# Performance work log

Measured on AMD Instinct MI355X. Metric: run time of the kernel, lower is better.

Reference implementation:

```python
import jax, jax.numpy as jnp
import numpy as np

D_MODEL = 64
HIDDEN = 64
N_HEADS = 4
HEAD_DIM = HIDDEN // N_HEADS  # 16
MAX_LEN = 128
LN_EPS = 1e-5


def setup_inputs() -> dict:
    key = jax.random.key(0)
    ks = jax.random.split(key, 16)
    B, Lh, Lp = 4096, 128, 32
    s = 0.02
    return {
        "hla_out": jax.random.normal(ks[0], (B, Lh, D_MODEL), jnp.float32),
        "pep_out": jax.random.normal(ks[1], (B, Lp, D_MODEL), jnp.float32),
        "W_hla": jax.random.normal(ks[2], (D_MODEL, HIDDEN), jnp.float32) * s,
        "b_hla": jnp.zeros((HIDDEN,), jnp.float32),
        "W_pep": jax.random.normal(ks[3], (D_MODEL, HIDDEN), jnp.float32) * s,
        "b_pep": jnp.zeros((HIDDEN,), jnp.float32),
        "rel_bias": jax.random.normal(ks[4], (N_HEADS, MAX_LEN, MAX_LEN), jnp.float32) * s,
        "ln_g": jnp.ones((HIDDEN,), jnp.float32),
        "ln_b": jnp.zeros((HIDDEN,), jnp.float32),
        "W1": jax.random.normal(ks[5], (HIDDEN, 2 * HIDDEN), jnp.float32) * s,
        "b1": jnp.zeros((2 * HIDDEN,), jnp.float32),
        "W2": jax.random.normal(ks[6], (2 * HIDDEN, HIDDEN), jnp.float32) * s,
        "b2": jnp.zeros((HIDDEN,), jnp.float32),
        "W_out": jax.random.normal(ks[7], (HIDDEN, D_MODEL), jnp.float32) * s,
        "b_out": jnp.zeros((D_MODEL,), jnp.float32),
    }


def _layernorm(x, g, b):
    mu = jnp.mean(x, axis=-1, keepdims=True)
    var = jnp.mean(jnp.square(x - mu), axis=-1, keepdims=True)
    return (x - mu) * jax.lax.rsqrt(var + LN_EPS) * g + b


def reference(hla_out, pep_out, W_hla, b_hla, W_pep, b_pep, rel_bias,
              ln_g, ln_b, W1, b1, W2, b2, W_out, b_out):
    B, Lh, _ = hla_out.shape
    Lp = pep_out.shape[1]
    hla = hla_out @ W_hla + b_hla              # [B, Lh, HIDDEN]
    pep = pep_out @ W_pep + b_pep              # [B, Lp, HIDDEN]
    q = hla.reshape(B, Lh, N_HEADS, HEAD_DIM)
    kv = pep.reshape(B, Lp, N_HEADS, HEAD_DIM)  # k and v share projection
    scale = 1.0 / np.sqrt(HEAD_DIM).astype(np.float32)
    # [B, H, Lh, Lp]
    scores = jnp.einsum('bqhd,bkhd->bhqk', q, kv) * scale
    scores = scores + rel_bias[:, :Lh, :Lp]
    attn = jax.nn.softmax(scores, axis=-1)
    ctx = jnp.einsum('bhqk,bkhd->bqhd', attn, kv).reshape(B, Lh, HIDDEN)
    h = _layernorm(ctx, ln_g, ln_b)
    h = jax.nn.gelu(h @ W1 + b1, approximate=False) @ W2 + b2
    hla2pep = hla + h                          # residual onto projected hla
    return hla2pep @ W_out + b_out             # [B, Lh, D_MODEL]
```

## Files before the change

kernel.cpp:

```cpp
#include <hip/hip_runtime.h>

#define DEV static __device__ __forceinline__

using bf16x8 = __attribute__((ext_vector_type(8))) short;
using f32x4  = __attribute__((ext_vector_type(4))) float;
using f32x16 = __attribute__((ext_vector_type(16))) float;
using bfp2   = __attribute__((ext_vector_type(2))) __bf16;
using u32x2  = __attribute__((ext_vector_type(2))) unsigned;

DEV unsigned short f2bf(float f){
  return __builtin_bit_cast(unsigned short, (__bf16)f);
}
DEV unsigned pk2(float a, float b){
  bfp2 v = {(__bf16)a, (__bf16)b};
  return __builtin_bit_cast(unsigned, v);
}
DEV void wr64(void* p, float a, float b, float c, float d){
  u32x2 v = {pk2(a, b), pk2(c, d)};
  *(u32x2*)p = v;
}

DEV float gelu_f(float x){
  float u = x * x;
  float c = __builtin_fmaf(u, 1.1543811e-4f, -1.1872348e-3f);
  c = __builtin_fmaf(u, c,  9.9735570e-3f);
  c = __builtin_fmaf(u, c, -6.6490380e-2f);
  c = __builtin_fmaf(u, c,  3.9894228e-1f);
  float t = __builtin_fmaf(x, c, 0.5f);
  return x * t;
}

__global__ void pack_weights(const float* __restrict__ Wh, const float* __restrict__ Wp,
                             const float* __restrict__ W1, const float* __restrict__ W2,
                             const float* __restrict__ Wo, const float* __restrict__ RB,
                             unsigned short* __restrict__ ws)
{
  const int gid = blockIdx.x * 256 + threadIdx.x;
  const float* W; unsigned short* o; int N, NB, idx;
  if      (gid < 4096)  { W = Wh; o = ws;         N = 64;  NB = 4; idx = gid;         }
  else if (gid < 8192)  { W = Wp; o = ws + 4096;  N = 64;  NB = 4; idx = gid - 4096;  }
  else if (gid < 16384) { W = W1; o = ws + 8192;  N = 128; NB = 8; idx = gid - 8192;  }
  else if (gid < 24576) { W = W2; o = ws + 16384; N = 64;  NB = 4; idx = gid - 16384; }
  else if (gid < 28672) { W = Wo; o = ws + 24576; N = 64;  NB = 4; idx = gid - 24576; }
  else {
    const int idx2 = gid - 28672;
    const int r = idx2 & 15, lx = (idx2 >> 4) & 63, fid = idx2 >> 10;
    const int qt = fid & 3, h = fid >> 2;
    const int q  = qt * 32 + (lx & 31);
    const int kp = (r & 3) + 8 * (r >> 2) + 4 * (lx >> 5);
    ((float*)(ws + 28672))[idx2] = 1.44269504f * RB[((size_t)h * 128 + q) * 128 + kp];
    return;
  }
  const int e = idx & 7, lx = (idx >> 3) & 63, fid = idx >> 9;
  const int kb = fid / NB, nb = fid % NB;
  const int k  = kb * 32 + ((lx >> 4) & 3) * 8 + e;
  const int n  = nb * 16 + (lx & 15);
  o[idx] = f2bf(W[k * N + n]);
}

#define KV_OFF  0
#define KVT_OFF 4608
#define SC_Q 0.36067376f

__global__ __launch_bounds__(256, 4)
void fused_kernel(const float* __restrict__ hla_in, const float* __restrict__ pep_in,
                  const float* __restrict__ bhla_p, const float* __restrict__ bpep_p,
                  const float* __restrict__ lng_p,  const float* __restrict__ lnb_p,
                  const float* __restrict__ b1_p,   const float* __restrict__ b2_p,
                  const float* __restrict__ bout_p,
                  const unsigned short* __restrict__ pk,
                  float* __restrict__ out)
{
  __shared__ __align__(16) unsigned char lds[38400];
  const int b   = blockIdx.x;
  const int tid = threadIdx.x;
  const int w   = tid >> 6;
  const int l   = tid & 63;
  const int li  = l & 15, l4 = l >> 4;
  const int lq  = l & 31, l5 = l >> 5;
  const int R0  = 32 * w;
  const unsigned QX = 9728u + (unsigned)w * 7168u;
  const unsigned PW = QX + 4608u;

  const unsigned short* pWh = pk;
  const unsigned short* pWp = pk + 4096;
  const unsigned short* pW1 = pk + 8192;
  const unsigned short* pW2 = pk + 16384;
  const unsigned short* pWo = pk + 24576;
  const float* pRBf = (const float*)(pk + 28672);

  {
    const int mt = w & 1, np = w >> 1;
    bf16x8 xP[2];
#pragma unroll
    for (int kb = 0; kb < 2; ++kb){
      const float* s = pep_in + ((size_t)b * 32 + 16 * mt + li) * 64 + kb * 32 + l4 * 8;
      f32x4 u0 = *(const f32x4*)s;
      f32x4 u1 = *(const f32x4*)(s + 4);
      bf16x8 a;
      a[0] = (short)f2bf(u0[0]); a[1] = (short)f2bf(u0[1]);
      a[2] = (short)f2bf(u0[2]); a[3] = (short)f2bf(u0[3]);
      a[4] = (short)f2bf(u1[0]); a[5] = (short)f2bf(u1[1]);
      a[6] = (short)f2bf(u1[2]); a[7] = (short)f2bf(u1[3]);
      xP[kb] = a;
    }
#pragma unroll
    for (int t = 0; t < 2; ++t){
      const int nt = 2 * np + t;
      f32x4 acc = *(const f32x4*)(bpep_p + nt * 16 + l4 * 4);
#pragma unroll
      for (int kb = 0; kb < 2; ++kb){
        bf16x8 wf = *(const bf16x8*)(pWp + (size_t)((kb * 4 + nt) * 64 + l) * 8);
        acc = __builtin_amdgcn_mfma_f32_16x16x32_bf16(wf, xP[kb], acc, 0, 0, 0);
      }
      wr64(lds + KV_OFF + (16 * mt + li) * 144 + (nt * 16 + l4 * 4) * 2,
           acc[0], acc[1], acc[2], acc[3]);
#pragma unroll
      for (int r = 0; r < 4; ++r)
        *(unsigned short*)(lds + KVT_OFF + (nt * 16 + l4 * 4 + r) * 80 + (16 * mt + li) * 2)
            = f2bf(acc[r]);
    }
  }

  f32x4 acc4[2][4];
  {
    bf16x8 xH[2][2];
#pragma unroll
    for (int ms = 0; ms < 2; ++ms)
#pragma unroll
    for (int kb = 0; kb < 2; ++kb){
      const float* s = hla_in + ((size_t)b * 128 + R0 + ms * 16 + li) * 64 + kb * 32 + l4 * 8;
      f32x4 u0 = *(const f32x4*)s;
      f32x4 u1 = *(const f32x4*)(s + 4);
      bf16x8 a;
      a[0] = (short)f2bf(u0[0]); a[1] = (short)f2bf(u0[1]);
      a[2] = (short)f2bf(u0[2]); a[3] = (short)f2bf(u0[3]);
      a[4] = (short)f2bf(u1[0]); a[5] = (short)f2bf(u1[1]);
      a[6] = (short)f2bf(u1[2]); a[7] = (short)f2bf(u1[3]);
      xH[ms][kb] = a;
    }
#pragma unroll
    for (int nt = 0; nt < 4; ++nt){
      f32x4 cin = *(const f32x4*)(bhla_p + nt * 16 + l4 * 4);
      f32x4 a0 = cin, a1 = cin;
#pragma unroll
      for (int kb = 0; kb < 2; ++kb){
        bf16x8 wf = *(const bf16x8*)(pWh + (size_t)((kb * 4 + nt) * 64 + l) * 8);
        a0 = __builtin_amdgcn_mfma_f32_16x16x32_bf16(wf, xH[0][kb], a0, 0, 0, 0);
        a1 = __builtin_amdgcn_mfma_f32_16x16x32_bf16(wf, xH[1][kb], a1, 0, 0, 0);
      }
      acc4[0][nt] = a0;
      acc4[1][nt] = a1;
      wr64(lds + QX + li * 144 + (nt * 16 + l4 * 4) * 2,
           a0[0] * SC_Q, a0[1] * SC_Q, a0[2] * SC_Q, a0[3] * SC_Q);
      wr64(lds + QX + (16 + li) * 144 + (nt * 16 + l4 * 4) * 2,
           a1[0] * SC_Q, a1[1] * SC_Q, a1[2] * SC_Q, a1[3] * SC_Q);
    }
  }

  __syncthreads();

  f32x4 ctxacc[2][4];
#pragma unroll
  for (int ms = 0; ms < 2; ++ms)
#pragma unroll
  for (int h = 0; h < 4; ++h){
    f32x4 z = {0.f, 0.f, 0.f, 0.f};
    ctxacc[ms][h] = z;
  }

#pragma unroll
  for (int h = 0; h < 4; ++h){
    bf16x8 kvA = *(const bf16x8*)(lds + KV_OFF + lq * 144 + h * 32 + l5 * 16);
    bf16x8 qB  = *(const bf16x8*)(lds + QX     + lq * 144 + h * 32 + l5 * 16);
    const f32x4* rp = (const f32x4*)(pRBf + (size_t)((h * 4 + w) * 64 + l) * 16);
    f32x4 c0 = rp[0], c1 = rp[1], c2 = rp[2], c3 = rp[3];
    f32x16 cc;
#pragma unroll
    for (int i = 0; i < 4; ++i){
      cc[i] = c0[i]; cc[4 + i] = c1[i]; cc[8 + i] = c2[i]; cc[12 + i] = c3[i];
    }
    f32x16 sc = __builtin_amdgcn_mfma_f32_32x32x16_bf16(kvA, qB, cc, 0, 0, 0);

    float p[16], sum = 0.f;
#pragma unroll
    for (int i = 0; i < 16; ++i){ p[i] = __builtin_amdgcn_exp2f(sc[i]); sum += p[i]; }
    sum += __shfl_xor(sum, 32);
    const float rs = __builtin_amdgcn_rcpf(sum);

#pragma unroll
    for (int qd = 0; qd < 4; ++qd)
      wr64(lds + PW + lq * 80 + (8 * qd + 4 * l5) * 2,
           p[4 * qd] * rs, p[4 * qd + 1] * rs, p[4 * qd + 2] * rs, p[4 * qd + 3] * rs);
    asm volatile("" ::: "memory");

    bf16x8 aV = *(const bf16x8*)(lds + KVT_OFF + (h * 16 + li) * 80 + l4 * 16);
#pragma unroll
    for (int ms = 0; ms < 2; ++ms){
      bf16x8 bP = *(const bf16x8*)(lds + PW + (ms * 16 + li) * 80 + l4 * 16);
      ctxacc[ms][h] = __builtin_amdgcn_mfma_f32_16x16x32_bf16(aV, bP, ctxacc[ms][h], 0, 0, 0);
    }
    asm volatile("" ::: "memory");
  }

  f32x4 gv[4], bv[4];
#pragma unroll
  for (int h = 0; h < 4; ++h){
    gv[h] = *(const f32x4*)(lng_p + h * 16 + l4 * 4);
    bv[h] = *(const f32x4*)(lnb_p + h * 16 + l4 * 4);
  }
#pragma unroll
  for (int ms = 0; ms < 2; ++ms){
    f32x4 s4 = ctxacc[ms][0] + ctxacc[ms][1] + ctxacc[ms][2] + ctxacc[ms][3];
    float s = s4[0] + s4[1] + s4[2] + s4[3];
    s += __shfl_xor(s, 16);
    s += __shfl_xor(s, 32);
    const float mean = s * 0.015625f;
    float q = 0.f;
#pragma unroll
    for (int h = 0; h < 4; ++h)
#pragma unroll
    for (int r = 0; r < 4; ++r) q = __builtin_fmaf(ctxacc[ms][h][r], ctxacc[ms][h][r], q);
    q += __shfl_xor(q, 16);
    q += __shfl_xor(q, 32);
    const float var  = __builtin_fmaf(mean, -mean, q * 0.015625f);
    const float rstd = __builtin_amdgcn_rsqf(var + 1e-5f);
#pragma unroll
    for (int h = 0; h < 4; ++h){
      f32x4 y;
#pragma unroll
      for (int r = 0; r < 4; ++r)
        y[r] = __builtin_fmaf((ctxacc[ms][h][r] - mean) * rstd, gv[h][r], bv[h][r]);
      wr64(lds + QX + (ms * 16 + li) * 144 + (h * 16 + l4 * 4) * 2, y[0], y[1], y[2], y[3]);
    }
  }
  asm volatile("" ::: "memory");

  bf16x8 xF[2][2];
#pragma unroll
  for (int ms = 0; ms < 2; ++ms)
#pragma unroll
  for (int kb = 0; kb < 2; ++kb)
    xF[ms][kb] = *(const bf16x8*)(lds + QX + (ms * 16 + li) * 144 + kb * 64 + l4 * 16);
  asm volatile("" ::: "memory");

#pragma unroll
  for (int half = 0; half < 2; ++half){
#pragma unroll
    for (int nt = 0; nt < 4; ++nt){
      f32x4 cin = *(const f32x4*)(b1_p + half * 64 + nt * 16 + l4 * 4);
      f32x4 h0 = cin, h1 = cin;
#pragma unroll
      for (int kb = 0; kb < 2; ++kb){
        bf16x8 wf = *(const bf16x8*)(pW1 + (size_t)((kb * 8 + half * 4 + nt) * 64 + l) * 8);
        h0 = __builtin_amdgcn_mfma_f32_16x16x32_bf16(wf, xF[0][kb], h0, 0, 0, 0);
        h1 = __builtin_amdgcn_mfma_f32_16x16x32_bf16(wf, xF[1][kb], h1, 0, 0, 0);
      }
      wr64(lds + QX + li * 144 + (nt * 16 + l4 * 4) * 2,
           gelu_f(h0[0]), gelu_f(h0[1]), gelu_f(h0[2]), gelu_f(h0[3]));
      wr64(lds + QX + (16 + li) * 144 + (nt * 16 + l4 * 4) * 2,
           gelu_f(h1[0]), gelu_f(h1[1]), gelu_f(h1[2]), gelu_f(h1[3]));
    }
    asm volatile("" ::: "memory");
    bf16x8 tF[2][2];
#pragma unroll
    for (int ms = 0; ms < 2; ++ms)
#pragma unroll
    for (int kb = 0; kb < 2; ++kb)
      tF[ms][kb] = *(const bf16x8*)(lds + QX + (ms * 16 + li) * 144 + kb * 64 + l4 * 16);
#pragma unroll
    for (int nt = 0; nt < 4; ++nt){
#pragma unroll
      for (int kb = 0; kb < 2; ++kb){
        bf16x8 wf = *(const bf16x8*)(pW2 + (size_t)(((half * 2 + kb) * 4 + nt) * 64 + l) * 8);
        acc4[0][nt] = __builtin_amdgcn_mfma_f32_16x16x32_bf16(wf, tF[0][kb], acc4[0][nt], 0, 0, 0);
        acc4[1][nt] = __builtin_amdgcn_mfma_f32_16x16x32_bf16(wf, tF[1][kb], acc4[1][nt], 0, 0, 0);
      }
    }
    asm volatile("" ::: "memory");
  }

#pragma unroll
  for (int nt = 0; nt < 4; ++nt){
    f32x4 b2v = *(const f32x4*)(b2_p + nt * 16 + l4 * 4);
#pragma unroll
    for (int ms = 0; ms < 2; ++ms){
      f32x4 v = acc4[ms][nt] + b2v;
      wr64(lds + QX + (ms * 16 + li) * 144 + (nt * 16 + l4 * 4) * 2, v[0], v[1], v[2], v[3]);
    }
  }
  asm volatile("" ::: "memory");

  bf16x8 rF[2][2];
#pragma unroll
  for (int ms = 0; ms < 2; ++ms)
#pragma unroll
  for (int kb = 0; kb < 2; ++kb)
    rF[ms][kb] = *(const bf16x8*)(lds + QX + (ms * 16 + li) * 144 + kb * 64 + l4 * 16);

#pragma unroll
  for (int nt = 0; nt < 4; ++nt){
    f32x4 cin = *(const f32x4*)(bout_p + nt * 16 + l4 * 4);
    f32x4 o0 = cin, o1 = cin;
#pragma unroll
    for (int kb = 0; kb < 2; ++kb){
      bf16x8 wf = *(const bf16x8*)(pWo + (size_t)((kb * 4 + nt) * 64 + l) * 8);
      o0 = __builtin_amdgcn_mfma_f32_16x16x32_bf16(wf, rF[0][kb], o0, 0, 0, 0);
      o1 = __builtin_amdgcn_mfma_f32_16x16x32_bf16(wf, rF[1][kb], o1, 0, 0, 0);
    }
    *(f32x4*)(out + ((size_t)b * 128 + R0 + li) * 64 + nt * 16 + l4 * 4)      = o0;
    *(f32x4*)(out + ((size_t)b * 128 + R0 + 16 + li) * 64 + nt * 16 + l4 * 4) = o1;
  }
}

extern "C" void kernel_launch(void* const* d_in, const int* in_sizes, int n_in,
                              void* d_out, int out_size, void* d_ws, size_t ws_size,
                              hipStream_t stream)
{
  const float* hla  = (const float*)d_in[0];
  const float* pep  = (const float*)d_in[1];
  const float* Wh   = (const float*)d_in[2];
  const float* bhla = (const float*)d_in[3];
  const float* Wp   = (const float*)d_in[4];
  const float* bpep = (const float*)d_in[5];
  const float* RB   = (const float*)d_in[6];
  const float* lng  = (const float*)d_in[7];
  const float* lnb  = (const float*)d_in[8];
  const float* W1   = (const float*)d_in[9];
  const float* b1   = (const float*)d_in[10];
  const float* W2   = (const float*)d_in[11];
  const float* b2   = (const float*)d_in[12];
  const float* Wo   = (const float*)d_in[13];
  const float* bo   = (const float*)d_in[14];
  unsigned short* ws = (unsigned short*)d_ws;
  float* outp = (float*)d_out;

  hipLaunchKernelGGL(pack_weights, dim3(176), dim3(256), 0, stream,
                     Wh, Wp, W1, W2, Wo, RB, ws);
  hipLaunchKernelGGL(fused_kernel, dim3(4096), dim3(256), 0, stream,
                     hla, pep, bhla, bpep, lng, lnb, b1, b2, bo, ws, outp);
}
```

Before: 319.2 us.

## Swizzle LDS rows, alias P buffer onto Q scratch, raise occupancy

Replaces the padded 144/80-byte LDS row strides with 128-byte rows using an XOR swizzle on 16-byte chunks. The per-wave softmax buffer is folded into the Q scratch region, and the one Q head that would be overwritten (h=1) is preloaded into registers. Together these shrink LDS from 38400 to 25600 bytes so launch bounds can ask for 6 blocks per CU instead of 4. The cost is higher register pressure under the tighter bound, and correctness depends on the P writes never clobbering Q columns still needed by later heads.

```diff
diff --git a/kernel.cpp b/kernel.cpp
--- a/kernel.cpp
+++ b/kernel.cpp
@@ -58,11 +58,16 @@
   o[idx] = f2bf(W[k * N + n]);
 }
 
-#define KV_OFF  0
-#define KVT_OFF 4608
+#define KV_OFF  0u
+#define KVT_OFF 4096u
+#define QX_BASE 9216u
 #define SC_Q 0.36067376f
 
-__global__ __launch_bounds__(256, 4)
+DEV unsigned qoff(unsigned base, unsigned row, unsigned byte){
+  return base + row * 128u + ((((byte >> 4) ^ (row & 7u)) & 7u) << 4) + (byte & 15u);
+}
+
+__global__ __launch_bounds__(256, 6)
 void fused_kernel(const float* __restrict__ hla_in, const float* __restrict__ pep_in,
                   const float* __restrict__ bhla_p, const float* __restrict__ bpep_p,
                   const float* __restrict__ lng_p,  const float* __restrict__ lnb_p,
@@ -71,7 +76,7 @@
                   const unsigned short* __restrict__ pk,
                   float* __restrict__ out)
 {
-  __shared__ __align__(16) unsigned char lds[38400];
+  __shared__ __align__(16) unsigned char lds[25600];
   const int b   = blockIdx.x;
   const int tid = threadIdx.x;
   const int w   = tid >> 6;
@@ -79,8 +84,7 @@
   const int li  = l & 15, l4 = l >> 4;
   const int lq  = l & 31, l5 = l >> 5;
   const int R0  = 32 * w;
-  const unsigned QX = 9728u + (unsigned)w * 7168u;
-  const unsigned PW = QX + 4608u;
+  const unsigned QX = QX_BASE + (unsigned)w * 4096u;
 
   const unsigned short* pWh = pk;
   const unsigned short* pWp = pk + 4096;
@@ -113,7 +117,7 @@
         bf16x8 wf = *(const bf16x8*)(pWp + (size_t)((kb * 4 + nt) * 64 + l) * 8);
         acc = __builtin_amdgcn_mfma_f32_16x16x32_bf16(wf, xP[kb], acc, 0, 0, 0);
       }
-      wr64(lds + KV_OFF + (16 * mt + li) * 144 + (nt * 16 + l4 * 4) * 2,
+      wr64(lds + qoff(KV_OFF, 16 * mt + li, 32 * nt + 8 * l4),
            acc[0], acc[1], acc[2], acc[3]);
 #pragma unroll
       for (int r = 0; r < 4; ++r)
@@ -151,9 +155,9 @@
       }
       acc4[0][nt] = a0;
       acc4[1][nt] = a1;
-      wr64(lds + QX + li * 144 + (nt * 16 + l4 * 4) * 2,
+      wr64(lds + qoff(QX, li, 32 * nt + 8 * l4),
            a0[0] * SC_Q, a0[1] * SC_Q, a0[2] * SC_Q, a0[3] * SC_Q);
-      wr64(lds + QX + (16 + li) * 144 + (nt * 16 + l4 * 4) * 2,
+      wr64(lds + qoff(QX, 16 + li, 32 * nt + 8 * l4),
            a1[0] * SC_Q, a1[1] * SC_Q, a1[2] * SC_Q, a1[3] * SC_Q);
     }
   }
@@ -169,10 +173,13 @@
     ctxacc[ms][h] = z;
   }
 
+  bf16x8 qB1 = *(const bf16x8*)(lds + qoff(QX, lq, 32 + 16 * l5));
+
 #pragma unroll
   for (int h = 0; h < 4; ++h){
-    bf16x8 kvA = *(const bf16x8*)(lds + KV_OFF + lq * 144 + h * 32 + l5 * 16);
-    bf16x8 qB  = *(const bf16x8*)(lds + QX     + lq * 144 + h * 32 + l5 * 16);
+    bf16x8 kvA = *(const bf16x8*)(lds + qoff(KV_OFF, lq, 32 * h + 16 * l5));
+    bf16x8 qB  = (h == 1) ? qB1
+               : *(const bf16x8*)(lds + qoff(QX, lq, 32 * h + 16 * l5));
     const f32x4* rp = (const f32x4*)(pRBf + (size_t)((h * 4 + w) * 64 + l) * 16);
     f32x4 c0 = rp[0], c1 = rp[1], c2 = rp[2], c3 = rp[3];
     f32x16 cc;
@@ -190,14 +197,14 @@
 
 #pragma unroll
     for (int qd = 0; qd < 4; ++qd)
-      wr64(lds + PW + lq * 80 + (8 * qd + 4 * l5) * 2,
+      wr64(lds + qoff(QX, lq, 16 * qd + 8 * l5),
            p[4 * qd] * rs, p[4 * qd + 1] * rs, p[4 * qd + 2] * rs, p[4 * qd + 3] * rs);
     asm volatile("" ::: "memory");
 
     bf16x8 aV = *(const bf16x8*)(lds + KVT_OFF + (h * 16 + li) * 80 + l4 * 16);
 #pragma unroll
     for (int ms = 0; ms < 2; ++ms){
-      bf16x8 bP = *(const bf16x8*)(lds + PW + (ms * 16 + li) * 80 + l4 * 16);
+      bf16x8 bP = *(const bf16x8*)(lds + qoff(QX, ms * 16 + li, l4 * 16));
       ctxacc[ms][h] = __builtin_amdgcn_mfma_f32_16x16x32_bf16(aV, bP, ctxacc[ms][h], 0, 0, 0);
     }
     asm volatile("" ::: "memory");
@@ -231,7 +238,7 @@
 #pragma unroll
       for (int r = 0; r < 4; ++r)
         y[r] = __builtin_fmaf((ctxacc[ms][h][r] - mean) * rstd, gv[h][r], bv[h][r]);
-      wr64(lds + QX + (ms * 16 + li) * 144 + (h * 16 + l4 * 4) * 2, y[0], y[1], y[2], y[3]);
+      wr64(lds + qoff(QX, ms * 16 + li, 32 * h + 8 * l4), y[0], y[1], y[2], y[3]);
     }
   }
   asm volatile("" ::: "memory");
@@ -241,7 +248,7 @@
   for (int ms = 0; ms < 2; ++ms)
 #pragma unroll
   for (int kb = 0; kb < 2; ++kb)
-    xF[ms][kb] = *(const bf16x8*)(lds + QX + (ms * 16 + li) * 144 + kb * 64 + l4 * 16);
+    xF[ms][kb] = *(const bf16x8*)(lds + qoff(QX, ms * 16 + li, 64 * kb + 16 * l4));
   asm volatile("" ::: "memory");
 
 #pragma unroll
@@ -256,9 +263,9 @@
         h0 = __builtin_amdgcn_mfma_f32_16x16x32_bf16(wf, xF[0][kb], h0, 0, 0, 0);
         h1 = __builtin_amdgcn_mfma_f32_16x16x32_bf16(wf, xF[1][kb], h1, 0, 0, 0);
       }
-      wr64(lds + QX + li * 144 + (nt * 16 + l4 * 4) * 2,
+      wr64(lds + qoff(QX, li, 32 * nt + 8 * l4),
            gelu_f(h0[0]), gelu_f(h0[1]), gelu_f(h0[2]), gelu_f(h0[3]));
-      wr64(lds + QX + (16 + li) * 144 + (nt * 16 + l4 * 4) * 2,
+      wr64(lds + qoff(QX, 16 + li, 32 * nt + 8 * l4),
            gelu_f(h1[0]), gelu_f(h1[1]), gelu_f(h1[2]), gelu_f(h1[3]));
     }
     asm volatile("" ::: "memory");
@@ -267,7 +274,7 @@
     for (int ms = 0; ms < 2; ++ms)
 #pragma unroll
     for (int kb = 0; kb < 2; ++kb)
-      tF[ms][kb] = *(const bf16x8*)(lds + QX + (ms * 16 + li) * 144 + kb * 64 + l4 * 16);
+      tF[ms][kb] = *(const bf16x8*)(lds + qoff(QX, ms * 16 + li, 64 * kb + 16 * l4));
 #pragma unroll
     for (int nt = 0; nt < 4; ++nt){
 #pragma unroll
@@ -286,7 +293,7 @@
 #pragma unroll
     for (int ms = 0; ms < 2; ++ms){
       f32x4 v = acc4[ms][nt] + b2v;
-      wr64(lds + QX + (ms * 16 + li) * 144 + (nt * 16 + l4 * 4) * 2, v[0], v[1], v[2], v[3]);
+      wr64(lds + qoff(QX, ms * 16 + li, 32 * nt + 8 * l4), v[0], v[1], v[2], v[3]);
     }
   }
   asm volatile("" ::: "memory");
@@ -296,7 +303,7 @@
   for (int ms = 0; ms < 2; ++ms)
 #pragma unroll
   for (int kb = 0; kb < 2; ++kb)
-    rF[ms][kb] = *(const bf16x8*)(lds + QX + (ms * 16 + li) * 144 + kb * 64 + l4 * 16);
+    rF[ms][kb] = *(const bf16x8*)(lds + qoff(QX, ms * 16 + li, 64 * kb + 16 * l4));
 
 #pragma unroll
   for (int nt = 0; nt < 4; ++nt){
```

After: 388.5 us. +21.7%, slower.
